# Optimization experiments

Measured on AMD Instinct MI355X. Metric: run time of the kernel, lower is better.

The kernel has to match this reference:

```python
import jax, jax.numpy as jnp
import numpy as np

NUM_HEADS = 8
NEG_INF = float(-2**32 + 1)
LN_EPS = 1e-8


def setup_inputs() -> dict:
    key = jax.random.key(0)
    ks = jax.random.split(key, 9)
    B, T, D = 4, 2048, 512
    inp = {
        "queries": jax.random.normal(ks[0], (B, T, D), jnp.float32),
        "keys": jax.random.normal(ks[1], (B, T, D), jnp.float32),
        "values": jax.random.normal(ks[2], (B, T, D), jnp.float32),
        "Wq": jax.random.normal(ks[3], (D, D), jnp.float32) / np.sqrt(D),
        "bq": jnp.zeros((D,), jnp.float32),
        "Wk": jax.random.normal(ks[4], (D, D), jnp.float32) / np.sqrt(D),
        "bk": jnp.zeros((D,), jnp.float32),
        "Wv": jax.random.normal(ks[5], (D, D), jnp.float32) / np.sqrt(D),
        "bv": jnp.zeros((D,), jnp.float32),
        "gamma": jnp.ones((D,), jnp.float32),
        "beta": jnp.zeros((D,), jnp.float32),
    }
    return inp


def _split_heads(x, h):
    # torch.cat(torch.chunk(x, h, dim=2), dim=0): [B,T,D] -> [h*B, T, D/h], head-major
    B, T, D = x.shape
    return x.reshape(B, T, h, D // h).transpose(2, 0, 1, 3).reshape(h * B, T, D // h)


def _merge_heads(x, h, B):
    # inverse: [h*B, T, dh] -> [B, T, h*dh]
    hB, T, dh = x.shape
    return x.reshape(h, B, T, dh).transpose(1, 2, 0, 3).reshape(B, T, h * dh)


def reference(queries, keys, values, Wq, bq, Wk, bk, Wv, bv, gamma, beta):
    h = NUM_HEADS
    B, Tq, D = queries.shape
    dh = D // h

    Q = jax.nn.relu(queries @ Wq + bq)
    K = jax.nn.relu(keys @ Wk + bk)
    V = jax.nn.relu(values @ Wv + bv)

    Q_ = _split_heads(Q, h)  # [h*B, Tq, dh]
    K_ = _split_heads(K, h)
    V_ = _split_heads(V, h)

    scores = jnp.einsum('bqd,bkd->bqk', Q_, K_) / jnp.sqrt(jnp.float32(dh))  # [h*B, Tq, Tk]

    # key padding mask: zero rows in `keys` get -inf scores
    key_mask = jnp.sign(jnp.abs(jnp.sum(keys, axis=-1)))  # [B, Tk]
    key_mask = jnp.tile(key_mask, (h, 1))  # [h*B, Tk]
    scores = jnp.where(key_mask[:, None, :] == 0.0, NEG_INF, scores)

    attn = jax.nn.softmax(scores, axis=-1)

    # query mask applied multiplicatively post-softmax
    query_mask = jnp.sign(jnp.abs(jnp.sum(queries, axis=-1)))  # [B, Tq]
    query_mask = jnp.tile(query_mask, (h, 1))  # [h*B, Tq]
    attn = attn * query_mask[:, :, None]

    out = jnp.einsum('bqk,bkd->bqd', attn, V_)  # [h*B, Tq, dh]
    out = _merge_heads(out, h, B) + queries  # residual

    # custom LayerNorm: torch.std is unbiased (ddof=1), eps added to std
    mean = out.mean(-1, keepdims=True)
    std = jnp.sqrt(out.var(-1, ddof=1, keepdims=True))
    return gamma * (out - mean) / (std + LN_EPS) + beta
```

## Files before the change

kernel.cpp:

```cpp
#include <hip/hip_runtime.h>


typedef __attribute__((ext_vector_type(8))) __bf16 bf16x8;
typedef __attribute__((ext_vector_type(4))) float f32x4;

#if __has_builtin(__builtin_amdgcn_exp2f)
#define EXP2F __builtin_amdgcn_exp2f
#else
#define EXP2F exp2f
#endif

#define QSCALE (0.125f * 1.4426950408889634f)

__device__ __forceinline__ unsigned short f2bf(float f) {
  return __builtin_bit_cast(unsigned short, (__bf16)f);
}
__device__ __forceinline__ unsigned pk2(float a, float b) {
  return (unsigned)f2bf(a) | ((unsigned)f2bf(b) << 16);
}
__device__ __forceinline__ f32x4 mfma16(bf16x8 a, bf16x8 b, f32x4 c) {
  return __builtin_amdgcn_mfma_f32_16x16x32_bf16(a, b, c, 0, 0, 0);
}
__device__ __forceinline__ bf16x8 ld_bf8(const unsigned short* p) {
  return *(const bf16x8*)p;
}
__device__ __forceinline__ void g2l16(const void* g, void* l) {
  __builtin_amdgcn_global_load_lds(
      (const __attribute__((address_space(1))) void*)g,
      (__attribute__((address_space(3))) void*)l, 16, 0, 0);
}

__global__ __launch_bounds__(256) void wt_kernel(const float* __restrict__ Wq,
                                                 const float* __restrict__ Wk,
                                                 const float* __restrict__ Wv,
                                                 unsigned short* __restrict__ Wt) {
  int idx = blockIdx.x * 256 + threadIdx.x;
  int o = idx * 8;
  int z = o >> 18;
  int rem = o & 262143;
  int n = rem >> 9;
  int k0 = rem & 511;
  const float* W = (z == 0) ? Wq : ((z == 1) ? Wk : Wv);
  unsigned int w[4];
#pragma unroll
  for (int i = 0; i < 4; ++i) {
    unsigned short lo = f2bf(W[(k0 + 2 * i) * 512 + n]);
    unsigned short hi = f2bf(W[(k0 + 2 * i + 1) * 512 + n]);
    w[i] = (unsigned)lo | ((unsigned)hi << 16);
  }
  *(uint4*)(Wt + o) = make_uint4(w[0], w[1], w[2], w[3]);
}

__global__ __launch_bounds__(256) void xcvt_kernel(
    const float* __restrict__ Xq, const float* __restrict__ Xk,
    const float* __restrict__ Xv, unsigned short* __restrict__ Xbq,
    unsigned short* __restrict__ Xbk, unsigned short* __restrict__ Xbv,
    float* __restrict__ qmask, float* __restrict__ kbias) {
  int row = blockIdx.x * 4 + (threadIdx.x >> 6);
  int lane = threadIdx.x & 63;
  int z = row >> 13;
  int r = row & 8191;
  const float* X = (z == 0) ? Xq : ((z == 1) ? Xk : Xv);
  unsigned short* Xb = (z == 0) ? Xbq : ((z == 1) ? Xbk : Xbv);
  const float* p = X + r * 512 + lane * 8;
  f32x4 lo = *(const f32x4*)p;
  f32x4 hi = *(const f32x4*)(p + 4);
  *(uint4*)(Xb + r * 512 + lane * 8) =
      make_uint4(pk2(lo[0], lo[1]), pk2(lo[2], lo[3]), pk2(hi[0], hi[1]),
                 pk2(hi[2], hi[3]));
  if (z < 2) {
    float s = lo[0] + lo[1] + lo[2] + lo[3] + hi[0] + hi[1] + hi[2] + hi[3];
#pragma unroll
    for (int off = 1; off < 64; off <<= 1) s += __shfl_xor(s, off);
    if (lane == 0) {
      if (z == 0)
        qmask[r] = (s == 0.f) ? 0.f : 1.f;
      else
        kbias[r] = (s == 0.f) ? -1.0e30f : 0.f;
    }
  }
}

__global__ __launch_bounds__(256, 3) void proj_kernel(
    const unsigned short* __restrict__ Xbq, const unsigned short* __restrict__ Xbk,
    const unsigned short* __restrict__ Xbv, const float* __restrict__ bq,
    const float* __restrict__ bk, const float* __restrict__ bv,
    const unsigned short* __restrict__ Wt, unsigned short* __restrict__ Qb,
    unsigned short* __restrict__ Kb, unsigned short* __restrict__ Vt) {
  __shared__ unsigned short Asm[2][128][32];
  __shared__ unsigned short Bsm[2][128][32];

  int tid = threadIdx.x;
  int m0g = blockIdx.x * 128;
  int z = m0g >> 13;
  int m0 = m0g & 8191;
  int n0 = blockIdx.y * 128;
  const unsigned short* Xb = (z == 0) ? Xbq : ((z == 1) ? Xbk : Xbv);
  const float* bias = (z == 0) ? bq : ((z == 1) ? bk : bv);
  const unsigned short* Wz = Wt + z * 262144;

  int w = tid >> 6, lane = tid & 63;
  int wm = w >> 1, wn = w & 1;
  int mrow = lane & 15, quad = lane >> 4;

  int srow = tid >> 2, sslot = tid & 3;
  int sxs = sslot ^ ((srow >> 1) & 3);
  const unsigned short* gA = Xb + (m0 + srow) * 512 + sxs * 8;
  const unsigned short* gB = Wz + (n0 + srow) * 512 + sxs * 8;
  char* lA = (char*)&Asm[0][0][0] + tid * 16;
  char* lB = (char*)&Bsm[0][0][0] + tid * 16;

  int rs = (quad ^ ((mrow >> 1) & 3)) * 8;

  f32x4 zero = {0.f, 0.f, 0.f, 0.f};
  f32x4 acc[4][4];
#pragma unroll
  for (int i = 0; i < 4; ++i)
#pragma unroll
    for (int j = 0; j < 4; ++j) acc[i][j] = zero;

  g2l16(gA, lA);
  g2l16(gA + 64 * 512, lA + 4096);
  g2l16(gB, lB);
  g2l16(gB + 64 * 512, lB + 4096);
  __syncthreads();

  for (int kc = 0; kc < 16; ++kc) {
    int cur = kc & 1;
    if (kc < 15) {
      int ko = (kc + 1) * 32;
      int nb = cur ^ 1;
      g2l16(gA + ko, lA + nb * 8192);
      g2l16(gA + ko + 64 * 512, lA + nb * 8192 + 4096);
      g2l16(gB + ko, lB + nb * 8192);
      g2l16(gB + ko + 64 * 512, lB + nb * 8192 + 4096);
    }
    bf16x8 af[4], bfr[4];
#pragma unroll
    for (int mt = 0; mt < 4; ++mt)
      af[mt] = ld_bf8(&Asm[cur][wm * 64 + mt * 16 + mrow][rs]);
#pragma unroll
    for (int nt = 0; nt < 4; ++nt)
      bfr[nt] = ld_bf8(&Bsm[cur][wn * 64 + nt * 16 + mrow][rs]);
#pragma unroll
    for (int mt = 0; mt < 4; ++mt)
#pragma unroll
      for (int nt = 0; nt < 4; ++nt)
        acc[mt][nt] = mfma16(af[mt], bfr[nt], acc[mt][nt]);
    __syncthreads();
  }

  if (z < 2) {
    unsigned short* dst = (z == 0) ? Qb : Kb;
    float sc = (z == 0) ? QSCALE : 1.0f;
#pragma unroll
    for (int nt = 0; nt < 4; ++nt) {
      int n = n0 + wn * 64 + nt * 16 + mrow;
      float bv_ = bias[n];
#pragma unroll
      for (int mt = 0; mt < 4; ++mt) {
        int m = m0 + wm * 64 + mt * 16 + quad * 4;
#pragma unroll
        for (int r = 0; r < 4; ++r) {
          float v = fmaxf(acc[mt][nt][r] + bv_, 0.f) * sc;
          dst[(m + r) * 512 + n] = f2bf(v);
        }
      }
    }
  } else {
#pragma unroll
    for (int nt = 0; nt < 4; ++nt) {
      int n = n0 + wn * 64 + nt * 16 + mrow;
      int hh = n >> 6, jj = n & 63;
      float bv_ = bias[n];
#pragma unroll
      for (int mt = 0; mt < 4; ++mt) {
        int grow = m0 + wm * 64 + mt * 16 + quad * 4;
        int bb = grow >> 11, tl = grow & 2047;
        int pos = (tl & ~31) + quad * 8 + (mt & 1) * 4;
        float p0 = fmaxf(acc[mt][nt][0] + bv_, 0.f);
        float p1 = fmaxf(acc[mt][nt][1] + bv_, 0.f);
        float p2 = fmaxf(acc[mt][nt][2] + bv_, 0.f);
        float p3 = fmaxf(acc[mt][nt][3] + bv_, 0.f);
        *(uint2*)(Vt + ((hh * 4 + bb) * 64 + jj) * 2048 + pos) =
            make_uint2(pk2(p0, p1), pk2(p2, p3));
      }
    }
  }
}

__global__ __launch_bounds__(512, 4) void attn_kernel(
    const unsigned short* __restrict__ Qb, const unsigned short* __restrict__ Kb,
    const unsigned short* __restrict__ Vt, const float* __restrict__ qmask,
    const float* __restrict__ kbias, const float* __restrict__ queries,
    float* __restrict__ out) {
  __shared__ char smem[65536];
  unsigned short* KsmS = (unsigned short*)smem;
  unsigned short* VsmS = (unsigned short*)(smem + 32768);

  int hb = blockIdx.x;
  int qt = blockIdx.y;
  int h = hb >> 2, b = hb & 3;
  int q0 = qt * 128;
  int tid = threadIdx.x;
  int w = tid >> 6, lane = tid & 63;
  int mrow = lane & 15, quad = lane >> 4;
  int mlow = mrow & 7;

  const unsigned short* gK =
      Kb + (b * 2048 + (tid >> 3)) * 512 + h * 64 + (((tid & 7) ^ ((tid >> 3) & 7)) * 8);
  const unsigned short* gV =
      Vt + (hb * 64 + (tid >> 4)) * 2048 + (((tid & 15) ^ ((tid >> 4) & 15)) * 8);

  bf16x8 qf0, qf1;
  {
    const unsigned short* qp =
        Qb + (b * 2048 + q0 + w * 16 + mrow) * 512 + h * 64 + quad * 8;
    qf0 = ld_bf8(qp);
    qf1 = ld_bf8(qp + 32);
  }

  bf16x8 onev;
#pragma unroll
  for (int i = 0; i < 8; ++i) onev[i] = (__bf16)1.0f;

  f32x4 zero = {0.f, 0.f, 0.f, 0.f};
  f32x4 oacc[4];
#pragma unroll
  for (int i = 0; i < 4; ++i) oacc[i] = zero;
  f32x4 lacc = zero;

  const float* kmB = kbias + b * 2048 + quad * 4;

  g2l16(gK, &KsmS[tid * 8]);
  g2l16(gK + 64 * 512, &KsmS[4096 + tid * 8]);
  g2l16(gV, &VsmS[tid * 8]);
  g2l16(gV + 32 * 2048, &VsmS[4096 + tid * 8]);

  for (int it = 0; it < 16; ++it) {
    int bi = it & 1;
    int kb = it * 128;
    __syncthreads();

    if (it < 15) {
      int nb = 1 - bi;
      int nkb = kb + 128;
      g2l16(gK + nkb * 512, &KsmS[nb * 8192 + tid * 8]);
      g2l16(gK + (nkb + 64) * 512, &KsmS[nb * 8192 + 4096 + tid * 8]);
      g2l16(gV + nkb, &VsmS[nb * 8192 + tid * 8]);
      g2l16(gV + nkb + 32 * 2048, &VsmS[nb * 8192 + 4096 + tid * 8]);
    }

    const unsigned short* Kc = KsmS + bi * 8192;
    const unsigned short* Vc = VsmS + bi * 8192;

#pragma unroll
    for (int g = 0; g < 4; ++g) {
      f32x4 km0 = *(const f32x4*)(kmB + kb + g * 32);
      f32x4 km1 = *(const f32x4*)(kmB + kb + g * 32 + 16);
      bf16x8 kf00 = ld_bf8(&Kc[(g * 32 + mrow) * 64 + ((quad) ^ mlow) * 8]);
      bf16x8 kf01 = ld_bf8(&Kc[(g * 32 + mrow) * 64 + ((4 + quad) ^ mlow) * 8]);
      bf16x8 kf10 = ld_bf8(&Kc[(g * 32 + 16 + mrow) * 64 + ((quad) ^ mlow) * 8]);
      bf16x8 kf11 = ld_bf8(&Kc[(g * 32 + 16 + mrow) * 64 + ((4 + quad) ^ mlow) * 8]);
      bf16x8 vfg[4];
#pragma unroll
      for (int dt = 0; dt < 4; ++dt)
        vfg[dt] = ld_bf8(&Vc[(dt * 16 + mrow) * 128 + ((g * 4 + quad) ^ mrow) * 8]);

      f32x4 s0 = mfma16(kf00, qf0, km0);
      s0 = mfma16(kf01, qf1, s0);
      f32x4 s1 = mfma16(kf10, qf0, km1);
      s1 = mfma16(kf11, qf1, s1);

      f32x4 p0, p1;
#pragma unroll
      for (int r = 0; r < 4; ++r) {
        p0[r] = EXP2F(s0[r]);
        p1[r] = EXP2F(s1[r]);
      }
      bf16x8 pf = __builtin_bit_cast(
          bf16x8, make_uint4(pk2(p0[0], p0[1]), pk2(p0[2], p0[3]),
                             pk2(p1[0], p1[1]), pk2(p1[2], p1[3])));
      lacc = mfma16(pf, onev, lacc);
#pragma unroll
      for (int dt = 0; dt < 4; ++dt)
        oacc[dt] = mfma16(pf, vfg[dt], oacc[dt]);
    }
  }

#pragma unroll
  for (int r = 0; r < 4; ++r) {
    int qg = b * 2048 + q0 + w * 16 + quad * 4 + r;
    float inv = qmask[qg] / lacc[r];
    const float* qsrc = queries + qg * 512 + h * 64 + mrow;
    float* od = out + qg * 512 + h * 64 + mrow;
#pragma unroll
    for (int dt = 0; dt < 4; ++dt)
      od[dt * 16] = oacc[dt][r] * inv + qsrc[dt * 16];
  }
}

__global__ __launch_bounds__(256) void ln_kernel(float* __restrict__ out,
                                                 const float* __restrict__ gamma,
                                                 const float* __restrict__ beta) {
  int row = blockIdx.x * 4 + (threadIdx.x >> 6);
  int lane = threadIdx.x & 63;
  float* p = out + row * 512;
  float4 v1 = ((const float4*)p)[lane];
  float4 v2 = ((const float4*)p)[64 + lane];
  float s = v1.x + v1.y + v1.z + v1.w + v2.x + v2.y + v2.z + v2.w;
  float sq = v1.x * v1.x + v1.y * v1.y + v1.z * v1.z + v1.w * v1.w +
             v2.x * v2.x + v2.y * v2.y + v2.z * v2.z + v2.w * v2.w;
#pragma unroll
  for (int off = 32; off > 0; off >>= 1) {
    s += __shfl_xor(s, off);
    sq += __shfl_xor(sq, off);
  }
  float mean = s * (1.f / 512.f);
  float var = fmaxf((sq - 512.f * mean * mean) * (1.f / 511.f), 0.f);
  float inv = 1.f / (sqrtf(var) + 1e-8f);
  float4 g1 = ((const float4*)gamma)[lane];
  float4 g2 = ((const float4*)gamma)[64 + lane];
  float4 b1 = ((const float4*)beta)[lane];
  float4 b2 = ((const float4*)beta)[64 + lane];
  v1.x = g1.x * (v1.x - mean) * inv + b1.x;
  v1.y = g1.y * (v1.y - mean) * inv + b1.y;
  v1.z = g1.z * (v1.z - mean) * inv + b1.z;
  v1.w = g1.w * (v1.w - mean) * inv + b1.w;
  v2.x = g2.x * (v2.x - mean) * inv + b2.x;
  v2.y = g2.y * (v2.y - mean) * inv + b2.y;
  v2.z = g2.z * (v2.z - mean) * inv + b2.z;
  v2.w = g2.w * (v2.w - mean) * inv + b2.w;
  ((float4*)p)[lane] = v1;
  ((float4*)p)[64 + lane] = v2;
}

extern "C" void kernel_launch(void* const* d_in, const int* in_sizes, int n_in,
                              void* d_out, int out_size, void* d_ws, size_t ws_size,
                              hipStream_t stream) {
  (void)in_sizes; (void)n_in; (void)out_size; (void)ws_size;
  const float* queries = (const float*)d_in[0];
  const float* keys    = (const float*)d_in[1];
  const float* values  = (const float*)d_in[2];
  const float* Wq = (const float*)d_in[3];
  const float* bq = (const float*)d_in[4];
  const float* Wk = (const float*)d_in[5];
  const float* bk = (const float*)d_in[6];
  const float* Wv = (const float*)d_in[7];
  const float* bv = (const float*)d_in[8];
  const float* gamma = (const float*)d_in[9];
  const float* beta  = (const float*)d_in[10];
  float* out = (float*)d_out;

  char* ws = (char*)d_ws;
  unsigned short* Qb = (unsigned short*)(ws);
  unsigned short* Kb = (unsigned short*)(ws + 8 * 1024 * 1024);
  unsigned short* Vt = (unsigned short*)(ws + 16 * 1024 * 1024);
  unsigned short* Wt = (unsigned short*)(ws + 24 * 1024 * 1024);
  unsigned short* Xbv = (unsigned short*)(ws + 26 * 1024 * 1024);
  float* qmask = (float*)(ws + 34 * 1024 * 1024);
  float* kbias = qmask + 8192;

  unsigned short* Xbq = (unsigned short*)d_out;
  unsigned short* Xbk = Xbq + 4194304;

  wt_kernel<<<384, 256, 0, stream>>>(Wq, Wk, Wv, Wt);
  xcvt_kernel<<<6144, 256, 0, stream>>>(queries, keys, values, Xbq, Xbk, Xbv,
                                        qmask, kbias);
  proj_kernel<<<dim3(192, 4), 256, 0, stream>>>(Xbq, Xbk, Xbv, bq, bk, bv,
                                                Wt, Qb, Kb, Vt);
  attn_kernel<<<dim3(32, 16), 512, 0, stream>>>(Qb, Kb, Vt, qmask, kbias,
                                                queries, out);
  ln_kernel<<<2048, 256, 0, stream>>>(out, gamma, beta);
}
```

Before: 190.0 us.

## Halve attention block threads, give each wave two query tiles, prefetch LDS fragments

```diff
diff --git a/kernel.cpp b/kernel.cpp
--- a/kernel.cpp
+++ b/kernel.cpp
@@ -189,7 +189,7 @@
   }
 }
 
-__global__ __launch_bounds__(512, 4) void attn_kernel(
+__global__ __launch_bounds__(256, 2) void attn_kernel(
     const unsigned short* __restrict__ Qb, const unsigned short* __restrict__ Kb,
     const unsigned short* __restrict__ Vt, const float* __restrict__ qmask,
     const float* __restrict__ kbias, const float* __restrict__ queries,
@@ -212,12 +212,15 @@
   const unsigned short* gV =
       Vt + (hb * 64 + (tid >> 4)) * 2048 + (((tid & 15) ^ ((tid >> 4) & 15)) * 8);
 
-  bf16x8 qf0, qf1;
+  bf16x8 qf[2][2];
   {
     const unsigned short* qp =
-        Qb + (b * 2048 + q0 + w * 16 + mrow) * 512 + h * 64 + quad * 8;
-    qf0 = ld_bf8(qp);
-    qf1 = ld_bf8(qp + 32);
+        Qb + (b * 2048 + q0 + w * 32 + mrow) * 512 + h * 64 + quad * 8;
+#pragma unroll
+    for (int qn = 0; qn < 2; ++qn) {
+      qf[qn][0] = ld_bf8(qp + qn * 8192);
+      qf[qn][1] = ld_bf8(qp + qn * 8192 + 32);
+    }
   }
 
   bf16x8 onev;
@@ -225,17 +228,20 @@
   for (int i = 0; i < 8; ++i) onev[i] = (__bf16)1.0f;
 
   f32x4 zero = {0.f, 0.f, 0.f, 0.f};
-  f32x4 oacc[4];
-#pragma unroll
-  for (int i = 0; i < 4; ++i) oacc[i] = zero;
-  f32x4 lacc = zero;
+  f32x4 oacc[4][2];
+#pragma unroll
+  for (int i = 0; i < 4; ++i)
+#pragma unroll
+    for (int j = 0; j < 2; ++j) oacc[i][j] = zero;
+  f32x4 lacc[2] = {zero, zero};
 
   const float* kmB = kbias + b * 2048 + quad * 4;
 
-  g2l16(gK, &KsmS[tid * 8]);
-  g2l16(gK + 64 * 512, &KsmS[4096 + tid * 8]);
-  g2l16(gV, &VsmS[tid * 8]);
-  g2l16(gV + 32 * 2048, &VsmS[4096 + tid * 8]);
+#pragma unroll
+  for (int j = 0; j < 4; ++j) {
+    g2l16(gK + j * 32 * 512, &KsmS[j * 2048 + tid * 8]);
+    g2l16(gV + j * 16 * 2048, &VsmS[j * 2048 + tid * 8]);
+  }
 
   for (int it = 0; it < 16; ++it) {
     int bi = it & 1;
@@ -245,58 +251,71 @@
     if (it < 15) {
       int nb = 1 - bi;
       int nkb = kb + 128;
-      g2l16(gK + nkb * 512, &KsmS[nb * 8192 + tid * 8]);
-      g2l16(gK + (nkb + 64) * 512, &KsmS[nb * 8192 + 4096 + tid * 8]);
-      g2l16(gV + nkb, &VsmS[nb * 8192 + tid * 8]);
-      g2l16(gV + nkb + 32 * 2048, &VsmS[nb * 8192 + 4096 + tid * 8]);
+#pragma unroll
+      for (int j = 0; j < 4; ++j) {
+        g2l16(gK + (nkb + j * 32) * 512, &KsmS[nb * 8192 + j * 2048 + tid * 8]);
+        g2l16(gV + nkb + j * 16 * 2048, &VsmS[nb * 8192 + j * 2048 + tid * 8]);
+      }
     }
 
     const unsigned short* Kc = KsmS + bi * 8192;
     const unsigned short* Vc = VsmS + bi * 8192;
 
+    bf16x8 kf[2][4], vf[2][4];
+    f32x4 km[2][2];
+    auto ldg = [&](int gi, int sl) {
+      km[sl][0] = *(const f32x4*)(kmB + kb + gi * 32);
+      km[sl][1] = *(const f32x4*)(kmB + kb + gi * 32 + 16);
+      kf[sl][0] = ld_bf8(&Kc[(gi * 32 + mrow) * 64 + (quad ^ mlow) * 8]);
+      kf[sl][1] = ld_bf8(&Kc[(gi * 32 + mrow) * 64 + ((4 + quad) ^ mlow) * 8]);
+      kf[sl][2] = ld_bf8(&Kc[(gi * 32 + 16 + mrow) * 64 + (quad ^ mlow) * 8]);
+      kf[sl][3] = ld_bf8(&Kc[(gi * 32 + 16 + mrow) * 64 + ((4 + quad) ^ mlow) * 8]);
+#pragma unroll
+      for (int dt = 0; dt < 4; ++dt)
+        vf[sl][dt] =
+            ld_bf8(&Vc[(dt * 16 + mrow) * 128 + ((gi * 4 + quad) ^ mrow) * 8]);
+    };
+
+    ldg(0, 0);
 #pragma unroll
     for (int g = 0; g < 4; ++g) {
-      f32x4 km0 = *(const f32x4*)(kmB + kb + g * 32);
-      f32x4 km1 = *(const f32x4*)(kmB + kb + g * 32 + 16);
-      bf16x8 kf00 = ld_bf8(&Kc[(g * 32 + mrow) * 64 + ((quad) ^ mlow) * 8]);
-      bf16x8 kf01 = ld_bf8(&Kc[(g * 32 + mrow) * 64 + ((4 + quad) ^ mlow) * 8]);
-      bf16x8 kf10 = ld_bf8(&Kc[(g * 32 + 16 + mrow) * 64 + ((quad) ^ mlow) * 8]);
-      bf16x8 kf11 = ld_bf8(&Kc[(g * 32 + 16 + mrow) * 64 + ((4 + quad) ^ mlow) * 8]);
-      bf16x8 vfg[4];
+      int cb = g & 1;
+      if (g < 3) ldg(g + 1, cb ^ 1);
+#pragma unroll
+      for (int qn = 0; qn < 2; ++qn) {
+        f32x4 s0 = mfma16(kf[cb][0], qf[qn][0], km[cb][0]);
+        s0 = mfma16(kf[cb][1], qf[qn][1], s0);
+        f32x4 s1 = mfma16(kf[cb][2], qf[qn][0], km[cb][1]);
+        s1 = mfma16(kf[cb][3], qf[qn][1], s1);
+        f32x4 p0, p1;
+#pragma unroll
+        for (int r = 0; r < 4; ++r) {
+          p0[r] = EXP2F(s0[r]);
+          p1[r] = EXP2F(s1[r]);
+        }
+        bf16x8 pf = __builtin_bit_cast(
+            bf16x8, make_uint4(pk2(p0[0], p0[1]), pk2(p0[2], p0[3]),
+                               pk2(p1[0], p1[1]), pk2(p1[2], p1[3])));
+        lacc[qn] = mfma16(pf, onev, lacc[qn]);
+#pragma unroll
+        for (int dt = 0; dt < 4; ++dt)
+          oacc[dt][qn] = mfma16(pf, vf[cb][dt], oacc[dt][qn]);
+      }
+    }
+  }
+
+#pragma unroll
+  for (int qn = 0; qn < 2; ++qn) {
+#pragma unroll
+    for (int r = 0; r < 4; ++r) {
+      int qg = b * 2048 + q0 + w * 32 + qn * 16 + quad * 4 + r;
+      float inv = qmask[qg] / lacc[qn][r];
+      const float* qsrc = queries + qg * 512 + h * 64 + mrow;
+      float* od = out + qg * 512 + h * 64 + mrow;
 #pragma unroll
       for (int dt = 0; dt < 4; ++dt)
-        vfg[dt] = ld_bf8(&Vc[(dt * 16 + mrow) * 128 + ((g * 4 + quad) ^ mrow) * 8]);
-
-      f32x4 s0 = mfma16(kf00, qf0, km0);
-      s0 = mfma16(kf01, qf1, s0);
-      f32x4 s1 = mfma16(kf10, qf0, km1);
-      s1 = mfma16(kf11, qf1, s1);
-
-      f32x4 p0, p1;
-#pragma unroll
-      for (int r = 0; r < 4; ++r) {
-        p0[r] = EXP2F(s0[r]);
-        p1[r] = EXP2F(s1[r]);
-      }
-      bf16x8 pf = __builtin_bit_cast(
-          bf16x8, make_uint4(pk2(p0[0], p0[1]), pk2(p0[2], p0[3]),
-                             pk2(p1[0], p1[1]), pk2(p1[2], p1[3])));
-      lacc = mfma16(pf, onev, lacc);
-#pragma unroll
-      for (int dt = 0; dt < 4; ++dt)
-        oacc[dt] = mfma16(pf, vfg[dt], oacc[dt]);
-    }
-  }
-
-#pragma unroll
-  for (int r = 0; r < 4; ++r) {
-    int qg = b * 2048 + q0 + w * 16 + quad * 4 + r;
-    float inv = qmask[qg] / lacc[r];
-    const float* qsrc = queries + qg * 512 + h * 64 + mrow;
-    float* od = out + qg * 512 + h * 64 + mrow;
-#pragma unroll
-    for (int dt = 0; dt < 4; ++dt)
-      od[dt * 16] = oacc[dt][r] * inv + qsrc[dt * 16];
+        od[dt * 16] = oacc[dt][qn][r] * inv + qsrc[dt * 16];
+    }
   }
 }
 
@@ -369,7 +388,7 @@
                                         qmask, kbias);
   proj_kernel<<<dim3(192, 4), 256, 0, stream>>>(Xbq, Xbk, Xbv, bq, bk, bv,
                                                 Wt, Qb, Kb, Vt);
-  attn_kernel<<<dim3(32, 16), 512, 0, stream>>>(Qb, Kb, Vt, qmask, kbias,
+  attn_kernel<<<dim3(32, 16), 256, 0, stream>>>(Qb, Kb, Vt, qmask, kbias,
                                                 queries, out);
   ln_kernel<<<2048, 256, 0, stream>>>(out, gamma, beta);
 }
```

After: 187.2 us. No clear change (-1.5%).
